# Performance work log

Measured on AMD Instinct MI355X. Metric: run time of the kernel, lower is better.

## Reference

```python
import jax, jax.numpy as jnp
import numpy as np

B, N, D = 2, 2048, 1024
H, ENC = 16, 8
HD = D // H
EPS = 1e-5


def _apply_rope(x, cos, sin):
    # x: [B,N,H,HD], cos/sin: [N,HD//2]
    c = cos[None, :, None, :]
    s = sin[None, :, None, :]
    x_re = x[..., 0::2]
    x_im = x[..., 1::2]
    out = jnp.stack([x_re * c - x_im * s, x_re * s + x_im * c], axis=-1)
    return out.reshape(x.shape)


def _rmsnorm(x):
    return x * jax.lax.rsqrt(jnp.mean(x * x, axis=-1, keepdims=True) + EPS)


def setup_inputs() -> dict:
    key = jax.random.key(0)
    ks = jax.random.split(key, 8)
    pos = jnp.arange(N, dtype=jnp.float32)[:, None]
    inv_freq = 1.0 / (10000.0 ** (jnp.arange(0, HD, 2, dtype=jnp.float32) / HD))  # [HD//2]
    ang = pos * inv_freq[None, :]
    std = 0.02
    return {
        "x": jax.random.normal(ks[0], (B, N, D), dtype=jnp.float32),
        "rope_cos": jnp.cos(ang),
        "rope_sin": jnp.sin(ang),
        "Wq": std * jax.random.normal(ks[1], (D, D), dtype=jnp.float32),
        "Wk": std * jax.random.normal(ks[2], (D, D), dtype=jnp.float32),
        "Wv": std * jax.random.normal(ks[3], (D, D), dtype=jnp.float32),
        "Wo_enc": std * jax.random.normal(ks[4], (H * HD, D), dtype=jnp.float32),
        "Wo_dec": std * jax.random.normal(ks[5], ((H - ENC) * HD, D), dtype=jnp.float32),
        "heads": H,
        "encoder_heads": ENC,
    }


def reference(x, rope_cos, rope_sin, Wq, Wk, Wv, Wo_enc, Wo_dec, heads, encoder_heads):
    b, n, d = x.shape
    hd = d // heads
    scale = hd ** (-0.5)
    q = (x @ Wq).reshape(b, n, heads, hd)
    k = (x @ Wk).reshape(b, n, heads, hd)
    v = (x @ Wv).reshape(b, n, heads, hd)
    q = _rmsnorm(_apply_rope(q, rope_cos, rope_sin))
    k = _rmsnorm(_apply_rope(k, rope_cos, rope_sin))
    # scores: [B,H,N,N]
    scores = jnp.einsum("bihd,bjhd->bhij", q, k) * scale
    causal = jnp.tril(jnp.ones((n, n), dtype=bool))  # [N,N]
    is_enc = (jnp.arange(heads) < encoder_heads)[:, None, None]  # [H,1,1]
    allow = jnp.logical_or(is_enc, causal[None, :, :])  # [H,N,N]
    scores = jnp.where(allow[None], scores, -jnp.inf)
    att = jax.nn.softmax(scores, axis=-1)
    out = jnp.einsum("bhij,bjhd->bihd", att, v)  # [B,N,H,HD]
    enc_out = out.reshape(b, n, heads * hd) @ Wo_enc
    dec_out = out[:, :, encoder_heads:, :].reshape(b, n, (heads - encoder_heads) * hd) @ Wo_dec
    return (enc_out, dec_out)
```

## Files before the change

kernel.cpp:

```cpp
#include <hip/hip_runtime.h>
#include <hip/hip_bf16.h>
#include <math.h>

#define B_    2
#define N_    2048
#define D_    1024
#define H_    16
#define ENC_  8
#define HD_   64
#define EPS_  1e-5f
#define M_    (B_ * N_)

typedef __bf16 bf16x8 __attribute__((ext_vector_type(8)));
typedef __bf16 bf16x2 __attribute__((ext_vector_type(2)));
typedef float  f32x4  __attribute__((ext_vector_type(4)));

#define MB(x) ((size_t)(x) * 1024 * 1024)

#define KSC_  0.18033688011112042f

#if __has_builtin(__builtin_amdgcn_exp2f)
#define EXP2F(x) __builtin_amdgcn_exp2f(x)
#else
#define EXP2F(x) exp2f(x)
#endif

__device__ __forceinline__ void gld16(const __bf16* g, __bf16* l) {
    __builtin_amdgcn_global_load_lds(
        (const __attribute__((address_space(1))) void*)g,
        (__attribute__((address_space(3))) void*)l,
        16, 0, 0);
}

template <typename OutT>
__device__ __forceinline__ void gemm_core(
    const __bf16* __restrict__ A, const __bf16* __restrict__ Bt,
    OutT* __restrict__ C, int K, int lda, int aoff, int ldc,
    int bm, int bn, __bf16* As, __bf16* Bs)
{
    const int tid  = threadIdx.x;
    const int w    = tid >> 6;
    const int lane = tid & 63;
    const int lrow = lane & 15;
    const int quad = lane >> 4;
    const int wr   = w >> 1;
    const int wc   = w & 1;

    const int sr = lane >> 2;
    const int sc = (lane & 3) * 8;
    const __bf16* Ag0 = A  + (size_t)(bm +      w * 16 + sr) * lda + aoff + sc;
    const __bf16* Ag1 = A  + (size_t)(bm + 64 + w * 16 + sr) * lda + aoff + sc;
    const __bf16* Bg0 = Bt + (size_t)(bn +      w * 16 + sr) * K + sc;
    const __bf16* Bg1 = Bt + (size_t)(bn + 64 + w * 16 + sr) * K + sc;
    __bf16* Al0 = &As[w * 512];
    __bf16* Al1 = &As[2048 + w * 512];
    __bf16* Bl0 = &Bs[w * 512];
    __bf16* Bl1 = &Bs[2048 + w * 512];

    f32x4 acc[4][4];
    #pragma unroll
    for (int i = 0; i < 4; ++i)
        #pragma unroll
        for (int j = 0; j < 4; ++j) acc[i][j] = (f32x4){0.f, 0.f, 0.f, 0.f};

    for (int k0 = 0; k0 < K; k0 += 32) {
        gld16(Ag0 + k0, Al0);
        gld16(Ag1 + k0, Al1);
        gld16(Bg0 + k0, Bl0);
        gld16(Bg1 + k0, Bl1);
        __syncthreads();

        bf16x8 af[4], bf[4];
        #pragma unroll
        for (int rt = 0; rt < 4; ++rt)
            af[rt] = *(const bf16x8*)&As[(wr * 64 + rt * 16 + lrow) * 32 + quad * 8];
        #pragma unroll
        for (int ct = 0; ct < 4; ++ct)
            bf[ct] = *(const bf16x8*)&Bs[(wc * 64 + ct * 16 + lrow) * 32 + quad * 8];

        #pragma unroll
        for (int rt = 0; rt < 4; ++rt)
            #pragma unroll
            for (int ct = 0; ct < 4; ++ct)
                acc[rt][ct] = __builtin_amdgcn_mfma_f32_16x16x32_bf16(
                    af[rt], bf[ct], acc[rt][ct], 0, 0, 0);
        __syncthreads();
    }

    #pragma unroll
    for (int rt = 0; rt < 4; ++rt)
        #pragma unroll
        for (int ct = 0; ct < 4; ++ct)
            #pragma unroll
            for (int r = 0; r < 4; ++r) {
                const int row = bm + wr * 64 + rt * 16 + quad * 4 + r;
                const int col = bn + wc * 64 + ct * 16 + lrow;
                C[(size_t)row * ldc + col] = (OutT)acc[rt][ct][r];
            }
}

__global__ __launch_bounds__(256) void gemm_qkv(
    const __bf16* __restrict__ A, const __bf16* __restrict__ Bt,
    __bf16* __restrict__ C)
{
    __shared__ __bf16 As[128 * 32];
    __shared__ __bf16 Bs[128 * 32];
    gemm_core<__bf16>(A, Bt, C, D_, D_, 0, 3072,
                      blockIdx.y * 128, blockIdx.x * 128, As, Bs);
}

__global__ __launch_bounds__(256) void gemm_out(
    const __bf16* __restrict__ A, const __bf16* __restrict__ Woe,
    const __bf16* __restrict__ Wod, float* __restrict__ Cenc,
    float* __restrict__ Cdec)
{
    __shared__ __bf16 As[128 * 32];
    __shared__ __bf16 Bs[128 * 32];
    const int bx = blockIdx.x;
    if (bx < 8) {
        gemm_core<float>(A, Woe, Cenc, 1024, D_, 0, D_,
                         blockIdx.y * 128, bx * 128, As, Bs);
    } else {
        gemm_core<float>(A, Wod, Cdec, 512, D_, 512, D_,
                         blockIdx.y * 128, (bx - 8) * 128, As, Bs);
    }
}

__global__ __launch_bounds__(256) void f32_to_bf16(
    const float* __restrict__ src, __bf16* __restrict__ dst)
{
    const size_t i = ((size_t)blockIdx.x * 256 + threadIdx.x) * 8;
    float4 a = *(const float4*)&src[i];
    float4 b = *(const float4*)&src[i + 4];
    bf16x8 o = {(__bf16)a.x, (__bf16)a.y, (__bf16)a.z, (__bf16)a.w,
                (__bf16)b.x, (__bf16)b.y, (__bf16)b.z, (__bf16)b.w};
    *(bf16x8*)&dst[i] = o;
}

struct WtArgs {
    const float* W[5];
    __bf16*      Wt[5];
    int          K[5];
    int          nyb[5];
};

__global__ __launch_bounds__(256) void wt_conv_all(WtArgs a)
{
    const int z = blockIdx.z;
    if (blockIdx.y >= a.nyb[z]) return;
    const float* W  = a.W[z];
    __bf16*      Wt = a.Wt[z];
    const int    K  = a.K[z];

    __shared__ __bf16 t[64][72];
    const int kb = blockIdx.y * 64;
    const int nb = blockIdx.x * 64;
    {
        const int kl = threadIdx.x >> 2;
        const int c0 = (threadIdx.x & 3) * 16;
        const float* src = W + (size_t)(kb + kl) * D_ + nb + c0;
        #pragma unroll
        for (int u = 0; u < 4; ++u) {
            float4 f = *(const float4*)&src[u * 4];
            t[c0 + u * 4 + 0][kl] = (__bf16)f.x;
            t[c0 + u * 4 + 1][kl] = (__bf16)f.y;
            t[c0 + u * 4 + 2][kl] = (__bf16)f.z;
            t[c0 + u * 4 + 3][kl] = (__bf16)f.w;
        }
    }
    __syncthreads();
    {
        const int nl  = threadIdx.x >> 2;
        const int k0c = (threadIdx.x & 3) * 16;
        __bf16* dst = Wt + (size_t)(nb + nl) * K + kb + k0c;
        *(bf16x8*)&dst[0] = *(const bf16x8*)&t[nl][k0c];
        *(bf16x8*)&dst[8] = *(const bf16x8*)&t[nl][k0c + 8];
    }
}

__global__ __launch_bounds__(256) void rope_vconv(
    const __bf16* __restrict__ qkv,
    const float* __restrict__ cs, const float* __restrict__ sn,
    __bf16* __restrict__ qbf, __bf16* __restrict__ kbf,
    __bf16* __restrict__ vt)
{
    if (blockIdx.x < 16384) {
        const int row  = blockIdx.x * 4 + (threadIdx.x >> 6);
        const int lane = threadIdx.x & 63;
        const int n    = (row >> 4) & (N_ - 1);
        const int b    = row >> 15;
        const int h    = row & 15;
        const int p    = lane >> 1;

        const float c = cs[n * (HD_ / 2) + p];
        const float s = sn[n * (HD_ / 2) + p];
        const size_t ibase = (size_t)(b * N_ + n) * 3072 + h * HD_ + lane;
        const size_t obase = ((size_t)(b * H_ + h) * N_ + n) * HD_ + lane;
        const bool odd = (lane & 1);

        {
            float val = (float)qkv[ibase];
            float partner = __shfl_xor(val, 1, 64);
            float r = odd ? fmaf(partner, s, val * c)
                          : (val * c - partner * s);
            float ss = r * r;
            #pragma unroll
            for (int off = 1; off < 64; off <<= 1) ss += __shfl_xor(ss, off, 64);
            qbf[obase] = (__bf16)(r * rsqrtf(ss * (1.0f / 64.0f) + EPS_) * KSC_);
        }
        {
            float val = (float)qkv[ibase + 1024];
            float partner = __shfl_xor(val, 1, 64);
            float r = odd ? fmaf(partner, s, val * c)
                          : (val * c - partner * s);
            float ss = r * r;
            #pragma unroll
            for (int off = 1; off < 64; off <<= 1) ss += __shfl_xor(ss, off, 64);
            kbf[obase] = (__bf16)(r * rsqrtf(ss * (1.0f / 64.0f) + EPS_));
        }
    } else {
        __shared__ __bf16 tile[64][72];
        const int bx = blockIdx.x - 16384;
        const int bh = bx >> 5;
        const int b  = bh >> 4, h = bh & 15;
        const int n0 = (bx & 31) * 64;
        {
            const int nl = threadIdx.x >> 2;
            const int d0 = (threadIdx.x & 3) * 16;
            const __bf16* src =
                qkv + (size_t)(b * N_ + n0 + nl) * 3072 + 2048 + h * HD_ + d0;
            bf16x8 v0 = *(const bf16x8*)&src[0];
            bf16x8 v1 = *(const bf16x8*)&src[8];
            #pragma unroll
            for (int e = 0; e < 8; ++e) {
                tile[d0 + e][nl]     = v0[e];
                tile[d0 + 8 + e][nl] = v1[e];
            }
        }
        __syncthreads();
        {
            const int dl = threadIdx.x >> 2;
            const int nc = (threadIdx.x & 3) * 16;
            __bf16* dst = vt + ((size_t)(bh * HD_ + dl)) * N_ + n0 + nc;
            bf16x8 o0, o1;
            #pragma unroll
            for (int e = 0; e < 8; ++e) {
                const int p0 = nc + e;
                const int p1 = nc + 8 + e;
                o0[e] = tile[dl][(p0 & ~31) + ((p0 & 31) >> 1) + 16 * (p0 & 1)];
                o1[e] = tile[dl][(p1 & ~31) + ((p1 & 31) >> 1) + 16 * (p1 & 1)];
            }
            *(bf16x8*)&dst[0] = o0;
            *(bf16x8*)&dst[8] = o1;
        }
    }
}

template <int NG, bool DEC>
__device__ __forceinline__ void attn_core(
    const __bf16* __restrict__ qbase, const __bf16* __restrict__ kbase,
    const __bf16* __restrict__ vbase, __bf16* __restrict__ o,
    int b, int h, int qb, int ntiles,
    __bf16 (*Ks)[4096], __bf16 (*Vs)[4096], __bf16* P)
{
    const int tid  = threadIdx.x;
    const int w    = tid >> 6;
    const int lane = tid & 63;
    const int lrow = lane & 15;
    const int quad = lane >> 4;

    const __bf16* kg0 = kbase + (size_t)lane * HD_ + w * 8;
    const __bf16* kg1 = kbase + (size_t)lane * HD_ + (w + 4) * 8;
    const __bf16* vg  = vbase + (size_t)lane * N_;

    int i0g[NG];
    #pragma unroll
    for (int g = 0; g < NG; ++g) i0g[g] = qb * (NG * 64) + g * 64 + w * 16;

    bf16x8 qf[NG][2];
    #pragma unroll
    for (int g = 0; g < NG; ++g)
        #pragma unroll
        for (int kc = 0; kc < 2; ++kc)
            qf[g][kc] = *(const bf16x8*)
                &qbase[(size_t)(i0g[g] + lrow) * HD_ + kc * 32 + quad * 8];

    const f32x4 zero = {0.f, 0.f, 0.f, 0.f};
    f32x4 oacc[NG][4];
    float lsum[NG][4];
    #pragma unroll
    for (int g = 0; g < NG; ++g)
        #pragma unroll
        for (int c = 0; c < 4; ++c) { oacc[g][c] = zero; lsum[g][c] = 0.f; }

    auto stage = [&](int t, int bb) {
        const int j0 = t << 6;
        gld16(kg0 + (size_t)j0 * HD_, &Ks[bb][(w)     * 512]);
        gld16(kg1 + (size_t)j0 * HD_, &Ks[bb][(w + 4) * 512]);
        gld16(vg + j0 + w * 8,        &Vs[bb][(w)     * 512]);
        gld16(vg + j0 + (w + 4) * 8,  &Vs[bb][(w + 4) * 512]);
    };

    stage(0, 0);
    for (int t = 0; t < ntiles; ++t) {
        const int bb = t & 1;
        __syncthreads();
        if (t + 1 < ntiles) stage(t + 1, bb ^ 1);

        #pragma unroll
        for (int s = 0; s < 2; ++s) {
            const int jp = (t << 6) + s * 32;

            bf16x8 kf0 = *(const bf16x8*)&Ks[bb][((quad)     * 64 + s * 32 + lrow) * 8];
            bf16x8 kf1 = *(const bf16x8*)&Ks[bb][((4 + quad) * 64 + s * 32 + lrow) * 8];
            bf16x8 kf2 = *(const bf16x8*)&Ks[bb][((quad)     * 64 + s * 32 + 16 + lrow) * 8];
            bf16x8 kf3 = *(const bf16x8*)&Ks[bb][((4 + quad) * 64 + s * 32 + 16 + lrow) * 8];

            f32x4 s0[NG], s1[NG];
            #pragma unroll
            for (int g = 0; g < NG; ++g) { s0[g] = zero; s1[g] = zero; }
            #pragma unroll
            for (int g = 0; g < NG; ++g)
                s0[g] = __builtin_amdgcn_mfma_f32_16x16x32_bf16(qf[g][0], kf0, s0[g], 0, 0, 0);
            #pragma unroll
            for (int g = 0; g < NG; ++g)
                s0[g] = __builtin_amdgcn_mfma_f32_16x16x32_bf16(qf[g][1], kf1, s0[g], 0, 0, 0);
            #pragma unroll
            for (int g = 0; g < NG; ++g)
                s1[g] = __builtin_amdgcn_mfma_f32_16x16x32_bf16(qf[g][0], kf2, s1[g], 0, 0, 0);
            #pragma unroll
            for (int g = 0; g < NG; ++g)
                s1[g] = __builtin_amdgcn_mfma_f32_16x16x32_bf16(qf[g][1], kf3, s1[g], 0, 0, 0);

            #pragma unroll
            for (int g = 0; g < NG; ++g) {
                __bf16* Pg = P + ((w * NG + g) * 16) * 36;
                if (DEC && (jp + 31 > i0g[g])) {
                    #pragma unroll
                    for (int r = 0; r < 4; ++r) {
                        const int i  = i0g[g] + quad * 4 + r;
                        float pA = (jp + lrow      <= i) ? EXP2F(s0[g][r]) : 0.f;
                        float pB = (jp + 16 + lrow <= i) ? EXP2F(s1[g][r]) : 0.f;
                        lsum[g][r] += pA + pB;
                        bf16x2 pp = {(__bf16)pA, (__bf16)pB};
                        *(bf16x2*)&Pg[(quad * 4 + r) * 36 + 2 * lrow] = pp;
                    }
                } else {
                    #pragma unroll
                    for (int r = 0; r < 4; ++r) {
                        float pA = EXP2F(s0[g][r]);
                        float pB = EXP2F(s1[g][r]);
                        lsum[g][r] += pA + pB;
                        bf16x2 pp = {(__bf16)pA, (__bf16)pB};
                        *(bf16x2*)&Pg[(quad * 4 + r) * 36 + 2 * lrow] = pp;
                    }
                }
            }

            bf16x8 vf0 = *(const bf16x8*)&Vs[bb][((s * 4 + quad) * 64 +  0 + lrow) * 8];
            bf16x8 vf1 = *(const bf16x8*)&Vs[bb][((s * 4 + quad) * 64 + 16 + lrow) * 8];
            bf16x8 vf2 = *(const bf16x8*)&Vs[bb][((s * 4 + quad) * 64 + 32 + lrow) * 8];
            bf16x8 vf3 = *(const bf16x8*)&Vs[bb][((s * 4 + quad) * 64 + 48 + lrow) * 8];

            bf16x8 pf[NG];
            #pragma unroll
            for (int g = 0; g < NG; ++g)
                pf[g] = *(const bf16x8*)&P[((w * NG + g) * 16 + lrow) * 36 + quad * 8];
            #pragma unroll
            for (int g = 0; g < NG; ++g) {
                oacc[g][0] = __builtin_amdgcn_mfma_f32_16x16x32_bf16(pf[g], vf0, oacc[g][0], 0, 0, 0);
                oacc[g][1] = __builtin_amdgcn_mfma_f32_16x16x32_bf16(pf[g], vf1, oacc[g][1], 0, 0, 0);
                oacc[g][2] = __builtin_amdgcn_mfma_f32_16x16x32_bf16(pf[g], vf2, oacc[g][2], 0, 0, 0);
                oacc[g][3] = __builtin_amdgcn_mfma_f32_16x16x32_bf16(pf[g], vf3, oacc[g][3], 0, 0, 0);
            }
        }
    }

    #pragma unroll
    for (int g = 0; g < NG; ++g)
        #pragma unroll
        for (int r = 0; r < 4; ++r) {
            float s = lsum[g][r];
            s += __shfl_xor(s, 1, 64);
            s += __shfl_xor(s, 2, 64);
            s += __shfl_xor(s, 4, 64);
            s += __shfl_xor(s, 8, 64);
            lsum[g][r] = 1.0f / s;
        }

    #pragma unroll
    for (int g = 0; g < NG; ++g)
        #pragma unroll
        for (int c = 0; c < 4; ++c)
            #pragma unroll
            for (int r = 0; r < 4; ++r) {
                const int i = i0g[g] + quad * 4 + r;
                o[(size_t)(b * N_ + i) * D_ + h * HD_ + c * 16 + lrow] =
                    (__bf16)(oacc[g][c][r] * lsum[g][r]);
            }
}

__global__ __launch_bounds__(256) void attn_mfma(
    const __bf16* __restrict__ qbf, const __bf16* __restrict__ kbf,
    const __bf16* __restrict__ vtbf, __bf16* __restrict__ o)
{
    __shared__ __bf16 Ks[2][4096];
    __shared__ __bf16 Vs[2][4096];
    __shared__ __bf16 P[4 * 2 * 16 * 36];

    if (blockIdx.x < 256) {
        const int e  = blockIdx.x & 15;
        const int bh = (e >> 3) * 16 + (e & 7);
        const int qb = blockIdx.x >> 4;
        attn_core<2, false>(
            qbf  + (size_t)bh * N_ * HD_, kbf + (size_t)bh * N_ * HD_,
            vtbf + (size_t)bh * HD_ * N_, o,
            bh >> 4, bh & 15, qb, N_ >> 6, Ks, Vs, P);
    } else {
        const int idx = blockIdx.x - 256;
        const int d   = idx & 15;
        const int bh  = (d >> 3) * 16 + 8 + (d & 7);
        const int qb  = 31 - (idx >> 4);
        attn_core<1, true>(
            qbf  + (size_t)bh * N_ * HD_, kbf + (size_t)bh * N_ * HD_,
            vtbf + (size_t)bh * HD_ * N_, o,
            bh >> 4, bh & 15, qb, qb + 1, Ks, Vs, P);
    }
}

extern "C" void kernel_launch(void* const* d_in, const int* in_sizes, int n_in,
                              void* d_out, int out_size, void* d_ws, size_t ws_size,
                              hipStream_t stream)
{
    const float* x   = (const float*)d_in[0];
    const float* cs  = (const float*)d_in[1];
    const float* sn  = (const float*)d_in[2];
    const float* Wq  = (const float*)d_in[3];
    const float* Wk  = (const float*)d_in[4];
    const float* Wv  = (const float*)d_in[5];
    const float* Woe = (const float*)d_in[6];
    const float* Wod = (const float*)d_in[7];

    float* enc_out = (float*)d_out;
    float* dec_out = enc_out + (size_t)M_ * D_;

    char* ws = (char*)d_ws;
    __bf16* xbf    = (__bf16*)(ws);
    __bf16* wqkv_t = (__bf16*)(ws + MB(8));
    __bf16* woe_t  = (__bf16*)(ws + MB(14));
    __bf16* wod_t  = (__bf16*)(ws + MB(16));
    __bf16* qkv    = (__bf16*)(ws + MB(17));
    __bf16* qbf    = (__bf16*)(ws + MB(41));
    __bf16* kbf    = (__bf16*)(ws + MB(49));
    __bf16* vtbf   = xbf;
    __bf16* obuf   = qkv;

    f32_to_bf16<<<(M_ * D_) / (256 * 8), 256, 0, stream>>>(x, xbf);

    WtArgs wa;
    wa.W[0] = Wq;  wa.Wt[0] = wqkv_t;                 wa.K[0] = 1024; wa.nyb[0] = 16;
    wa.W[1] = Wk;  wa.Wt[1] = wqkv_t + 1024 * 1024;   wa.K[1] = 1024; wa.nyb[1] = 16;
    wa.W[2] = Wv;  wa.Wt[2] = wqkv_t + 2048 * 1024;   wa.K[2] = 1024; wa.nyb[2] = 16;
    wa.W[3] = Woe; wa.Wt[3] = woe_t;                  wa.K[3] = 1024; wa.nyb[3] = 16;
    wa.W[4] = Wod; wa.Wt[4] = wod_t;                  wa.K[4] = 512;  wa.nyb[4] = 8;
    wt_conv_all<<<dim3(16, 16, 5), 256, 0, stream>>>(wa);

    gemm_qkv<<<dim3(3072 / 128, M_ / 128), 256, 0, stream>>>(xbf, wqkv_t, qkv);

    rope_vconv<<<16384 + 1024, 256, 0, stream>>>(qkv, cs, sn, qbf, kbf, vtbf);

    attn_mfma<<<dim3(768), 256, 0, stream>>>(qbf, kbf, vtbf, obuf);

    gemm_out<<<dim3(16, M_ / 128), 256, 0, stream>>>(
        obuf, woe_t, wod_t, enc_out, dec_out);
}
```

Baseline: 237.2 us.

## Compute transposed scores so P stays in registers, dropping LDS round-trip

Swaps the MFMA operand order so each lane holds scores for one query row across keys, letting the exponentiated probabilities be packed directly into the bf16x8 A-operand of the PV MFMA. Removes the shared-memory P buffer and its write/read per sub-tile. The V-transpose permutation is changed to match the new key ordering, and the row-sum reduction now runs across quads with a broadcast shuffle. This relies on the permuted V layout being consistent with the new P register layout.

```diff
diff --git a/kernel.cpp b/kernel.cpp
--- a/kernel.cpp
+++ b/kernel.cpp
@@ -247,8 +247,10 @@
             for (int e = 0; e < 8; ++e) {
                 const int p0 = nc + e;
                 const int p1 = nc + 8 + e;
-                o0[e] = tile[dl][(p0 & ~31) + ((p0 & 31) >> 1) + 16 * (p0 & 1)];
-                o1[e] = tile[dl][(p1 & ~31) + ((p1 & 31) >> 1) + 16 * (p1 & 1)];
+                o0[e] = tile[dl][(p0 & ~31) + (((p0 >> 2) & 1) << 4)
+                                 + (((p0 >> 3) & 3) << 2) + (p0 & 3)];
+                o1[e] = tile[dl][(p1 & ~31) + (((p1 >> 2) & 1) << 4)
+                                 + (((p1 >> 3) & 3) << 2) + (p1 & 3)];
             }
             *(bf16x8*)&dst[0] = o0;
             *(bf16x8*)&dst[8] = o1;
@@ -261,7 +263,7 @@
     const __bf16* __restrict__ qbase, const __bf16* __restrict__ kbase,
     const __bf16* __restrict__ vbase, __bf16* __restrict__ o,
     int b, int h, int qb, int ntiles,
-    __bf16 (*Ks)[4096], __bf16 (*Vs)[4096], __bf16* P)
+    __bf16 (*Ks)[4096], __bf16 (*Vs)[4096])
 {
     const int tid  = threadIdx.x;
     const int w    = tid >> 6;
@@ -287,11 +289,13 @@
 
     const f32x4 zero = {0.f, 0.f, 0.f, 0.f};
     f32x4 oacc[NG][4];
-    float lsum[NG][4];
-    #pragma unroll
-    for (int g = 0; g < NG; ++g)
-        #pragma unroll
-        for (int c = 0; c < 4; ++c) { oacc[g][c] = zero; lsum[g][c] = 0.f; }
+    float lsum[NG];
+    #pragma unroll
+    for (int g = 0; g < NG; ++g) {
+        lsum[g] = 0.f;
+        #pragma unroll
+        for (int c = 0; c < 4; ++c) oacc[g][c] = zero;
+    }
 
     auto stage = [&](int t, int bb) {
         const int j0 = t << 6;
@@ -321,40 +325,42 @@
             for (int g = 0; g < NG; ++g) { s0[g] = zero; s1[g] = zero; }
             #pragma unroll
             for (int g = 0; g < NG; ++g)
-                s0[g] = __builtin_amdgcn_mfma_f32_16x16x32_bf16(qf[g][0], kf0, s0[g], 0, 0, 0);
+                s0[g] = __builtin_amdgcn_mfma_f32_16x16x32_bf16(kf0, qf[g][0], s0[g], 0, 0, 0);
             #pragma unroll
             for (int g = 0; g < NG; ++g)
-                s0[g] = __builtin_amdgcn_mfma_f32_16x16x32_bf16(qf[g][1], kf1, s0[g], 0, 0, 0);
+                s0[g] = __builtin_amdgcn_mfma_f32_16x16x32_bf16(kf1, qf[g][1], s0[g], 0, 0, 0);
             #pragma unroll
             for (int g = 0; g < NG; ++g)
-                s1[g] = __builtin_amdgcn_mfma_f32_16x16x32_bf16(qf[g][0], kf2, s1[g], 0, 0, 0);
+                s1[g] = __builtin_amdgcn_mfma_f32_16x16x32_bf16(kf2, qf[g][0], s1[g], 0, 0, 0);
             #pragma unroll
             for (int g = 0; g < NG; ++g)
-                s1[g] = __builtin_amdgcn_mfma_f32_16x16x32_bf16(qf[g][1], kf3, s1[g], 0, 0, 0);
-
+                s1[g] = __builtin_amdgcn_mfma_f32_16x16x32_bf16(kf3, qf[g][1], s1[g], 0, 0, 0);
+
+            bf16x8 pf[NG];
             #pragma unroll
             for (int g = 0; g < NG; ++g) {
-                __bf16* Pg = P + ((w * NG + g) * 16) * 36;
+                float pA[4], pB[4];
                 if (DEC && (jp + 31 > i0g[g])) {
+                    const int i = i0g[g] + lrow;
                     #pragma unroll
                     for (int r = 0; r < 4; ++r) {
-                        const int i  = i0g[g] + quad * 4 + r;
-                        float pA = (jp + lrow      <= i) ? EXP2F(s0[g][r]) : 0.f;
-                        float pB = (jp + 16 + lrow <= i) ? EXP2F(s1[g][r]) : 0.f;
-                        lsum[g][r] += pA + pB;
-                        bf16x2 pp = {(__bf16)pA, (__bf16)pB};
-                        *(bf16x2*)&Pg[(quad * 4 + r) * 36 + 2 * lrow] = pp;
+                        const int k0 = jp + quad * 4 + r;
+                        pA[r] = (k0      <= i) ? EXP2F(s0[g][r]) : 0.f;
+                        pB[r] = (k0 + 16 <= i) ? EXP2F(s1[g][r]) : 0.f;
                     }
                 } else {
                     #pragma unroll
                     for (int r = 0; r < 4; ++r) {
-                        float pA = EXP2F(s0[g][r]);
-                        float pB = EXP2F(s1[g][r]);
-                        lsum[g][r] += pA + pB;
-                        bf16x2 pp = {(__bf16)pA, (__bf16)pB};
-                        *(bf16x2*)&Pg[(quad * 4 + r) * 36 + 2 * lrow] = pp;
+                        pA[r] = EXP2F(s0[g][r]);
+                        pB[r] = EXP2F(s1[g][r]);
                     }
                 }
+                lsum[g] += (pA[0] + pA[1]) + (pA[2] + pA[3])
+                         + (pB[0] + pB[1]) + (pB[2] + pB[3]);
+                pf[g] = (bf16x8){(__bf16)pA[0], (__bf16)pA[1],
+                                 (__bf16)pA[2], (__bf16)pA[3],
+                                 (__bf16)pB[0], (__bf16)pB[1],
+                                 (__bf16)pB[2], (__bf16)pB[3]};
             }
 
             bf16x8 vf0 = *(const bf16x8*)&Vs[bb][((s * 4 + quad) * 64 +  0 + lrow) * 8];
@@ -362,10 +368,6 @@
             bf16x8 vf2 = *(const bf16x8*)&Vs[bb][((s * 4 + quad) * 64 + 32 + lrow) * 8];
             bf16x8 vf3 = *(const bf16x8*)&Vs[bb][((s * 4 + quad) * 64 + 48 + lrow) * 8];
 
-            bf16x8 pf[NG];
-            #pragma unroll
-            for (int g = 0; g < NG; ++g)
-                pf[g] = *(const bf16x8*)&P[((w * NG + g) * 16 + lrow) * 36 + quad * 8];
             #pragma unroll
             for (int g = 0; g < NG; ++g) {
                 oacc[g][0] = __builtin_amdgcn_mfma_f32_16x16x32_bf16(pf[g], vf0, oacc[g][0], 0, 0, 0);
@@ -376,17 +378,17 @@
         }
     }
 
-    #pragma unroll
-    for (int g = 0; g < NG; ++g)
-        #pragma unroll
-        for (int r = 0; r < 4; ++r) {
-            float s = lsum[g][r];
-            s += __shfl_xor(s, 1, 64);
-            s += __shfl_xor(s, 2, 64);
-            s += __shfl_xor(s, 4, 64);
-            s += __shfl_xor(s, 8, 64);
-            lsum[g][r] = 1.0f / s;
-        }
+    float lrec[NG][4];
+    #pragma unroll
+    for (int g = 0; g < NG; ++g) {
+        float s = lsum[g];
+        s += __shfl_xor(s, 16, 64);
+        s += __shfl_xor(s, 32, 64);
+        s = 1.0f / s;
+        #pragma unroll
+        for (int r = 0; r < 4; ++r)
+            lrec[g][r] = __shfl(s, quad * 4 + r, 64);
+    }
 
     #pragma unroll
     for (int g = 0; g < NG; ++g)
@@ -396,7 +398,7 @@
             for (int r = 0; r < 4; ++r) {
                 const int i = i0g[g] + quad * 4 + r;
                 o[(size_t)(b * N_ + i) * D_ + h * HD_ + c * 16 + lrow] =
-                    (__bf16)(oacc[g][c][r] * lsum[g][r]);
+                    (__bf16)(oacc[g][c][r] * lrec[g][r]);
             }
 }
 
@@ -406,7 +408,6 @@
 {
     __shared__ __bf16 Ks[2][4096];
     __shared__ __bf16 Vs[2][4096];
-    __shared__ __bf16 P[4 * 2 * 16 * 36];
 
     if (blockIdx.x < 256) {
         const int e  = blockIdx.x & 15;
@@ -415,7 +416,7 @@
         attn_core<2, false>(
             qbf  + (size_t)bh * N_ * HD_, kbf + (size_t)bh * N_ * HD_,
             vtbf + (size_t)bh * HD_ * N_, o,
-            bh >> 4, bh & 15, qb, N_ >> 6, Ks, Vs, P);
+            bh >> 4, bh & 15, qb, N_ >> 6, Ks, Vs);
     } else {
         const int idx = blockIdx.x - 256;
         const int d   = idx & 15;
@@ -424,7 +425,7 @@
         attn_core<1, true>(
             qbf  + (size_t)bh * N_ * HD_, kbf + (size_t)bh * N_ * HD_,
             vtbf + (size_t)bh * HD_ * N_, o,
-            bh >> 4, bh & 15, qb, qb + 1, Ks, Vs, P);
+            bh >> 4, bh & 15, qb, qb + 1, Ks, Vs);
     }
 }
 
```

After: 222.7 us. 1.07x faster.
